# Kernel tuning notes

Hardware: AMD Instinct MI355X
Metric: run time of the kernel (lower is better)

## Reference

```python
import jax, jax.numpy as jnp
import numpy as np

# Static discretization grid (torch version computes this on host from data;
# with inputs in [0,1) the clamps min(..,-2)-0.1 / max(..,2)+0.1 make it constant).
PPU = 128          # points_per_unit
MULT = 16          # 2 ** rho.num_halving_layers
XMIN, XMAX = -2.1, 2.1
NUM_GRID = int(np.ceil(PPU * (XMAX - XMIN) / MULT) * MULT)  # 544
SIGMA_CH = 1024
RHO_C = 8          # rho in/out channels


def setup_inputs() -> dict:
    key = jax.random.key(0)
    ks = jax.random.split(key, 8)
    B, N, M = 8, 2048, 2048
    log_ls = float(np.log(2.0 / PPU))  # init_length_scale = 2 / points_per_unit
    return {
        "x": jax.random.uniform(ks[0], (B, N, 1), dtype=jnp.float32),
        "y": jax.random.normal(ks[1], (B, N, 1), dtype=jnp.float32),
        "x_out": jax.random.uniform(ks[2], (B, M, 1), dtype=jnp.float32),
        # encoder ConvDeepSet (in_channels = 2: density + y)
        "enc_sigma": jnp.full((2,), log_ls, dtype=jnp.float32),
        "enc_W": jax.random.normal(ks[3], (2, RHO_C), dtype=jnp.float32) * 0.5,
        "enc_b": jnp.zeros((RHO_C,), dtype=jnp.float32),
        # rho stand-in: point-wise linear 8 -> 8
        "rho_W": jax.random.normal(ks[4], (RHO_C, RHO_C), dtype=jnp.float32) * 0.35,
        "rho_b": jnp.zeros((RHO_C,), dtype=jnp.float32),
        # mean FinalLayer (in_channels = rho.out_channels = 8, out_channels = 1)
        "mean_sigma": jnp.full((RHO_C,), log_ls, dtype=jnp.float32),
        "mean_W": jax.random.normal(ks[5], (RHO_C, 1), dtype=jnp.float32) * 0.35,
        "mean_b": jnp.zeros((1,), dtype=jnp.float32),
        # sigma FinalLayer (out_channels = sigma_channels = 1024)
        "sig_sigma": jnp.full((RHO_C,), log_ls, dtype=jnp.float32),
        "sig_W": jax.random.normal(ks[6], (RHO_C, SIGMA_CH), dtype=jnp.float32) * 0.35,
        "sig_b": jnp.zeros((SIGMA_CH,), dtype=jnp.float32),
        "noise_scale": jnp.zeros((1,), dtype=jnp.float32),
    }


def _rbf_weights(a, t, log_sigma):
    # a: (B, n, 1), t: (B, m, 1) -> (B, n, m, C) per-channel RBF weights
    d = (a - jnp.swapaxes(t, 1, 2)) ** 2            # (B, n, m) squared dists
    scales = jnp.exp(log_sigma)                      # (C,)
    return jnp.exp(-0.5 * d[..., None] / scales ** 2)


def reference(x, y, x_out, enc_sigma, enc_W, enc_b, rho_W, rho_b,
              mean_sigma, mean_W, mean_b, sig_sigma, sig_W, sig_b, noise_scale):
    B = x.shape[0]
    grid = jnp.broadcast_to(
        jnp.linspace(XMIN, XMAX, NUM_GRID, dtype=x.dtype)[None, :, None],
        (B, NUM_GRID, 1))

    # --- encoder ConvDeepSet: density channel + value channel, RBF smoothing onto grid
    wt = _rbf_weights(x, grid, enc_sigma)            # (B, N, G, 2)
    y_aug = jnp.concatenate([jnp.ones_like(x), y], axis=-1)  # (B, N, 2)
    F = jnp.einsum('bnc,bngc->bgc', y_aug, wt)       # (B, G, 2)
    den, conv = F[..., :1], F[..., 1:]
    F = jnp.concatenate([den, conv / (den + 1e-8)], axis=-1)
    h = jax.nn.sigmoid(F @ enc_W + enc_b)            # (B, G, 8)

    # --- rho (stand-in point-wise linear CNN)
    h = h @ rho_W + rho_b                            # (B, G, 8)

    # --- mean FinalLayer: RBF set-conv from grid to x_out, then linear
    wt_m = _rbf_weights(grid, x_out, mean_sigma)     # (B, G, M, 8)
    mean = jnp.einsum('bgc,bgmc->bmc', h, wt_m) @ mean_W + mean_b  # (B, M, 1)

    # --- sigma FinalLayer -> basis embedding, inner-product covariance
    wt_s = _rbf_weights(grid, x_out, sig_sigma)      # (B, G, M, 8)
    basis = jnp.einsum('bgc,bgmc->bmc', h, wt_s) @ sig_W + sig_b   # (B, M, 1024)
    cov = jnp.einsum('bmc,bnc->bmn', basis, basis)   # (B, M, M)
    cov = cov + jnp.exp(noise_scale[0]) * jnp.eye(cov.shape[-1], dtype=cov.dtype)
    return mean, cov
```

## Files before the change

kernel.cpp:

```cpp
#include <hip/hip_runtime.h>
#include <math.h>

#define GRID_N 544
#define BATCH  8
#define NPTS   2048
#define MPTS   2048
#define XMIN_F (-2.1f)
#define STEP_F (4.2f / 543.0f)

#define PRM_OFF 0
#define H_OFF   128
#define FS_OFF  (H_OFF + BATCH*GRID_N*8)
#define P_OFF   (FS_OFF + BATCH*MPTS*8)
#define CM_OFF  (P_OFF + BATCH*MPTS*8)

__global__ __launch_bounds__(256) void k_params(
    const float* __restrict__ enc_sigma, const float* __restrict__ mean_sigma,
    const float* __restrict__ sig_sigma, const float* __restrict__ sig_W,
    const float* __restrict__ sig_b, const float* __restrict__ noise_scale,
    float* __restrict__ prm) {
  int t = threadIdx.x;
  __shared__ float part[256];
  {
    int pair = t >> 2, q = t & 3;
    int i = pair >> 3, j = pair & 7;
    float s = 0.f;
    int k0 = q * 256;
    for (int k = k0; k < k0 + 256; ++k) s += sig_W[i*1024+k] * sig_W[j*1024+k];
    part[t] = s;
    __syncthreads();
    if (q == 0) prm[24 + pair] = part[t] + part[t+1] + part[t+2] + part[t+3];
    __syncthreads();
  }
  {
    int ch = t >> 5, lane = t & 31;
    float s = 0.f;
    for (int k = lane; k < 1024; k += 32) s += sig_W[ch*1024+k] * sig_b[k];
    part[t] = s;
    __syncthreads();
    if (lane == 0) {
      float acc = 0.f;
      for (int k = 0; k < 32; ++k) acc += part[(ch<<5)+k];
      prm[88 + ch] = acc;
    }
    __syncthreads();
  }
  if (t < 32) {
    float v = 0.f;
    for (int k = t; k < 1024; k += 32) v += sig_b[k] * sig_b[k];
    part[t] = v;
  }
  __syncthreads();
  if (t == 0) {
    float v = 0.f;
    for (int k = 0; k < 32; ++k) v += part[k];
    prm[96] = v;
    prm[97] = __expf(noise_scale[0]);
  } else if (t == 1) {
    prm[0] = 0.5f * __expf(-2.f * enc_sigma[0]);
    prm[1] = 0.5f * __expf(-2.f * enc_sigma[1]);
    prm[98] = (enc_sigma[0] == enc_sigma[1]) ? 1.f : 0.f;
    bool mu = true, su = true;
    for (int c = 0; c < 8; ++c) {
      prm[8 + c]  = 0.5f * __expf(-2.f * mean_sigma[c]);
      prm[16 + c] = 0.5f * __expf(-2.f * sig_sigma[c]);
      if (mean_sigma[c] != mean_sigma[0]) mu = false;
      if (sig_sigma[c]  != sig_sigma[0])  su = false;
    }
    prm[99]  = mu ? 1.f : 0.f;
    prm[100] = su ? 1.f : 0.f;
    prm[101] = (mu && su && mean_sigma[0] == sig_sigma[0]) ? 1.f : 0.f;
  }
}

__global__ __launch_bounds__(256) void k_encode(
    const float* __restrict__ x, const float* __restrict__ y,
    const float* __restrict__ enc_W, const float* __restrict__ enc_b,
    const float* __restrict__ rho_W, const float* __restrict__ rho_b,
    const float* __restrict__ prm, float* __restrict__ h_out) {
  int b = blockIdx.y, g = blockIdx.x, t = threadIdx.x;
  float gv = XMIN_F + (float)g * STEP_F;
  float a0 = prm[0], a1 = prm[1];
  bool uni = prm[98] != 0.f;
  const float4* x4 = (const float4*)(x + (size_t)b * NPTS);
  const float4* y4 = (const float4*)(y + (size_t)b * NPTS);
  float s0 = 0.f, s1 = 0.f;
  #pragma unroll
  for (int i = 0; i < 2; ++i) {
    int n = i * 256 + t;
    float4 xv = x4[n], yv = y4[n];
    float dx, d, w;
    dx = xv.x - gv; d = dx*dx; w = __expf(-d*a0); s0 += w;
    s1 += yv.x * (uni ? w : __expf(-d*a1));
    dx = xv.y - gv; d = dx*dx; w = __expf(-d*a0); s0 += w;
    s1 += yv.y * (uni ? w : __expf(-d*a1));
    dx = xv.z - gv; d = dx*dx; w = __expf(-d*a0); s0 += w;
    s1 += yv.z * (uni ? w : __expf(-d*a1));
    dx = xv.w - gv; d = dx*dx; w = __expf(-d*a0); s0 += w;
    s1 += yv.w * (uni ? w : __expf(-d*a1));
  }
  #pragma unroll
  for (int off = 32; off > 0; off >>= 1) {
    s0 += __shfl_down(s0, off);
    s1 += __shfl_down(s1, off);
  }
  __shared__ float w0s[4], w1s[4];
  int wid = t >> 6;
  if ((t & 63) == 0) { w0s[wid] = s0; w1s[wid] = s1; }
  __syncthreads();
  if (t == 0) {
    float den = w0s[0] + w0s[1] + w0s[2] + w0s[3];
    float conv = w1s[0] + w1s[1] + w1s[2] + w1s[3];
    float F0 = den, F1 = conv / (den + 1e-8f);
    float hh[8];
    #pragma unroll
    for (int jj = 0; jj < 8; ++jj) {
      float z = F0 * enc_W[jj] + F1 * enc_W[8 + jj] + enc_b[jj];
      hh[jj] = 1.f / (1.f + __expf(-z));
    }
    #pragma unroll
    for (int jj = 0; jj < 8; ++jj) {
      float v = rho_b[jj];
      #pragma unroll
      for (int ii = 0; ii < 8; ++ii) v += hh[ii] * rho_W[ii*8 + jj];
      h_out[((size_t)b * GRID_N + g) * 8 + jj] = v;
    }
  }
}

__global__ __launch_bounds__(256) void k_feat(
    const float* __restrict__ x_out, const float* __restrict__ mean_W,
    const float* __restrict__ mean_b, const float* __restrict__ prm,
    const float* __restrict__ h, float* __restrict__ mean_out,
    float* __restrict__ fS, float* __restrict__ Pv, float* __restrict__ cm) {
  int b = blockIdx.y, t = threadIdx.x;
  int ml = t & 63, slice = t >> 6;
  int m = blockIdx.x * 64 + ml;
  float xo = x_out[(size_t)b * MPTS + m];
  bool fused = prm[101] != 0.f;
  float accm[8] = {0,0,0,0,0,0,0,0};
  float accs[8] = {0,0,0,0,0,0,0,0};
  const float* hb = h + (size_t)b * GRID_N * 8;
  const float4* h4 = (const float4*)hb;
  int gbase = slice * 136;
  if (fused) {
    float a = prm[8];
    for (int gg = 0; gg < 136; ++gg) {
      int g = gbase + gg;
      float gv = XMIN_F + (float)g * STEP_F;
      float dx = gv - xo;
      float w = __expf(-(dx*dx) * a);
      float4 h0 = h4[g*2], h1 = h4[g*2+1];
      accm[0] += h0.x * w; accm[1] += h0.y * w;
      accm[2] += h0.z * w; accm[3] += h0.w * w;
      accm[4] += h1.x * w; accm[5] += h1.y * w;
      accm[6] += h1.z * w; accm[7] += h1.w * w;
    }
    #pragma unroll
    for (int c = 0; c < 8; ++c) accs[c] = accm[c];
  } else {
    float am[8], asg[8];
    #pragma unroll
    for (int c = 0; c < 8; ++c) { am[c] = prm[8 + c]; asg[c] = prm[16 + c]; }
    for (int gg = 0; gg < 136; ++gg) {
      int g = gbase + gg;
      float gv = XMIN_F + (float)g * STEP_F;
      float dx = gv - xo;
      float d = dx * dx;
      #pragma unroll
      for (int c = 0; c < 8; ++c) {
        float hv = hb[g*8 + c];
        accm[c] += hv * __expf(-d * am[c]);
        accs[c] += hv * __expf(-d * asg[c]);
      }
    }
  }
  __shared__ float red[256 * 17];
  #pragma unroll
  for (int c = 0; c < 8; ++c) { red[t*17 + c] = accm[c]; red[t*17 + 8 + c] = accs[c]; }
  __syncthreads();
  if (t < 64) {
    int mm = blockIdx.x * 64 + t;
    float fm[8], fs[8];
    #pragma unroll
    for (int c = 0; c < 8; ++c) {
      fm[c] = red[t*17+c] + red[(t+64)*17+c] + red[(t+128)*17+c] + red[(t+192)*17+c];
      fs[c] = red[t*17+8+c] + red[(t+64)*17+8+c] + red[(t+128)*17+8+c] + red[(t+192)*17+8+c];
    }
    float mv = mean_b[0];
    #pragma unroll
    for (int c = 0; c < 8; ++c) mv += fm[c] * mean_W[c];
    mean_out[(size_t)b * MPTS + mm] = mv;
    float cmv = prm[96];
    #pragma unroll
    for (int c = 0; c < 8; ++c) cmv += fs[c] * prm[88 + c];
    cm[(size_t)b * MPTS + mm] = cmv;
    size_t base = ((size_t)b * MPTS + mm) * 8;
    #pragma unroll
    for (int c2 = 0; c2 < 8; ++c2) {
      float p = prm[88 + c2];
      #pragma unroll
      for (int c = 0; c < 8; ++c) p += fs[c] * prm[24 + c*8 + c2];
      Pv[base + c2] = p;
    }
    #pragma unroll
    for (int c = 0; c < 8; ++c) fS[base + c] = fs[c];
  }
}

__global__ __launch_bounds__(256) void k_cov(
    const float* __restrict__ fS, const float* __restrict__ Pv,
    const float* __restrict__ cm, const float* __restrict__ prm,
    float* __restrict__ cov) {
  int b = blockIdx.y, t = threadIdx.x;
  int mt = blockIdx.x * 16;
  int n0 = t * 8;
  float fn[8][8];
  const float4* fv = (const float4*)(fS + ((size_t)b * MPTS + n0) * 8);
  #pragma unroll
  for (int j = 0; j < 8; ++j) {
    float4 lo = fv[j*2], hi = fv[j*2+1];
    fn[j][0]=lo.x; fn[j][1]=lo.y; fn[j][2]=lo.z; fn[j][3]=lo.w;
    fn[j][4]=hi.x; fn[j][5]=hi.y; fn[j][6]=hi.z; fn[j][7]=hi.w;
  }
  __shared__ float Ps[16*8];
  __shared__ float Cs[16];
  if (t < 128) Ps[t] = Pv[((size_t)b * MPTS + mt) * 8 + t];
  if (t < 16)  Cs[t] = cm[(size_t)b * MPTS + mt + t];
  float noise = prm[97];
  __syncthreads();
  #pragma unroll 1
  for (int mi = 0; mi < 16; ++mi) {
    float p[8];
    #pragma unroll
    for (int c = 0; c < 8; ++c) p[c] = Ps[mi*8 + c];
    float cc = Cs[mi];
    float o[8];
    #pragma unroll
    for (int j = 0; j < 8; ++j) {
      float acc = cc;
      #pragma unroll
      for (int c = 0; c < 8; ++c) acc += p[c] * fn[j][c];
      o[j] = acc;
    }
    int mg = mt + mi;
    if (mg >= n0 && mg < n0 + 8) o[mg - n0] += noise;
    float4* outp = (float4*)(cov + ((size_t)b * MPTS + mg) * MPTS + n0);
    outp[0] = make_float4(o[0], o[1], o[2], o[3]);
    outp[1] = make_float4(o[4], o[5], o[6], o[7]);
  }
}

extern "C" void kernel_launch(void* const* d_in, const int* in_sizes, int n_in,
                              void* d_out, int out_size, void* d_ws, size_t ws_size,
                              hipStream_t stream) {
  const float* x          = (const float*)d_in[0];
  const float* y          = (const float*)d_in[1];
  const float* x_out      = (const float*)d_in[2];
  const float* enc_sigma  = (const float*)d_in[3];
  const float* enc_W      = (const float*)d_in[4];
  const float* enc_b      = (const float*)d_in[5];
  const float* rho_W      = (const float*)d_in[6];
  const float* rho_b      = (const float*)d_in[7];
  const float* mean_sigma = (const float*)d_in[8];
  const float* mean_W     = (const float*)d_in[9];
  const float* mean_b     = (const float*)d_in[10];
  const float* sig_sigma  = (const float*)d_in[11];
  const float* sig_W      = (const float*)d_in[12];
  const float* sig_b      = (const float*)d_in[13];
  const float* noise_sc   = (const float*)d_in[14];

  float* wsf = (float*)d_ws;
  float* prm = wsf + PRM_OFF;
  float* hbuf = wsf + H_OFF;
  float* fSb = wsf + FS_OFF;
  float* Pb  = wsf + P_OFF;
  float* cmb = wsf + CM_OFF;

  float* mean_out = (float*)d_out;
  float* cov_out  = mean_out + (size_t)BATCH * MPTS;

  k_params<<<1, 256, 0, stream>>>(enc_sigma, mean_sigma, sig_sigma,
                                  sig_W, sig_b, noise_sc, prm);
  k_encode<<<dim3(GRID_N, BATCH), 256, 0, stream>>>(x, y, enc_W, enc_b,
                                                    rho_W, rho_b, prm, hbuf);
  k_feat<<<dim3(MPTS/64, BATCH), 256, 0, stream>>>(x_out, mean_W, mean_b, prm,
                                                   hbuf, mean_out, fSb, Pb, cmb);
  k_cov<<<dim3(MPTS/16, BATCH), 256, 0, stream>>>(fSb, Pb, cmb, prm, cov_out);
}
```

Before: 221.9 us.

## Fold params kernel into encode, split feat grid finer, coalesce cov row stores

Removes the single-block k_params launch by computing its work in an extra block of k_encode, and computes encoder scales inline. k_feat now uses 32 outputs per block with 8 grid slices, doubling the block count, and skips writing the duplicate sigma partial sums when the bandwidths match. k_cov changes each thread's columns from 8 contiguous to two groups of 4 so that float4 row stores are coalesced across threads. The main cost targeted is the store pattern of the large covariance output, plus one kernel launch. In exchange there is a small register-layout change and a k_feat reduction with more partial sums.

```diff
diff --git a/kernel.cpp b/kernel.cpp
--- a/kernel.cpp
+++ b/kernel.cpp
@@ -14,74 +14,71 @@
 #define P_OFF   (FS_OFF + BATCH*MPTS*8)
 #define CM_OFF  (P_OFF + BATCH*MPTS*8)
 
-__global__ __launch_bounds__(256) void k_params(
-    const float* __restrict__ enc_sigma, const float* __restrict__ mean_sigma,
-    const float* __restrict__ sig_sigma, const float* __restrict__ sig_W,
-    const float* __restrict__ sig_b, const float* __restrict__ noise_scale,
-    float* __restrict__ prm) {
-  int t = threadIdx.x;
-  __shared__ float part[256];
-  {
-    int pair = t >> 2, q = t & 3;
-    int i = pair >> 3, j = pair & 7;
-    float s = 0.f;
-    int k0 = q * 256;
-    for (int k = k0; k < k0 + 256; ++k) s += sig_W[i*1024+k] * sig_W[j*1024+k];
-    part[t] = s;
-    __syncthreads();
-    if (q == 0) prm[24 + pair] = part[t] + part[t+1] + part[t+2] + part[t+3];
-    __syncthreads();
-  }
-  {
-    int ch = t >> 5, lane = t & 31;
-    float s = 0.f;
-    for (int k = lane; k < 1024; k += 32) s += sig_W[ch*1024+k] * sig_b[k];
-    part[t] = s;
-    __syncthreads();
-    if (lane == 0) {
-      float acc = 0.f;
-      for (int k = 0; k < 32; ++k) acc += part[(ch<<5)+k];
-      prm[88 + ch] = acc;
-    }
-    __syncthreads();
-  }
-  if (t < 32) {
-    float v = 0.f;
-    for (int k = t; k < 1024; k += 32) v += sig_b[k] * sig_b[k];
-    part[t] = v;
-  }
-  __syncthreads();
-  if (t == 0) {
-    float v = 0.f;
-    for (int k = 0; k < 32; ++k) v += part[k];
-    prm[96] = v;
-    prm[97] = __expf(noise_scale[0]);
-  } else if (t == 1) {
-    prm[0] = 0.5f * __expf(-2.f * enc_sigma[0]);
-    prm[1] = 0.5f * __expf(-2.f * enc_sigma[1]);
-    prm[98] = (enc_sigma[0] == enc_sigma[1]) ? 1.f : 0.f;
-    bool mu = true, su = true;
-    for (int c = 0; c < 8; ++c) {
-      prm[8 + c]  = 0.5f * __expf(-2.f * mean_sigma[c]);
-      prm[16 + c] = 0.5f * __expf(-2.f * sig_sigma[c]);
-      if (mean_sigma[c] != mean_sigma[0]) mu = false;
-      if (sig_sigma[c]  != sig_sigma[0])  su = false;
-    }
-    prm[99]  = mu ? 1.f : 0.f;
-    prm[100] = su ? 1.f : 0.f;
-    prm[101] = (mu && su && mean_sigma[0] == sig_sigma[0]) ? 1.f : 0.f;
-  }
-}
-
 __global__ __launch_bounds__(256) void k_encode(
     const float* __restrict__ x, const float* __restrict__ y,
+    const float* __restrict__ enc_sigma,
     const float* __restrict__ enc_W, const float* __restrict__ enc_b,
     const float* __restrict__ rho_W, const float* __restrict__ rho_b,
-    const float* __restrict__ prm, float* __restrict__ h_out) {
+    const float* __restrict__ mean_sigma, const float* __restrict__ sig_sigma,
+    const float* __restrict__ sig_W, const float* __restrict__ sig_b,
+    float* __restrict__ prm, float* __restrict__ h_out) {
   int b = blockIdx.y, g = blockIdx.x, t = threadIdx.x;
+
+  if (g == GRID_N) {
+    if (b != 0) return;
+    __shared__ float part[256];
+    {
+      int pair = t >> 2, q = t & 3;
+      int i = pair >> 3, j = pair & 7;
+      float s = 0.f;
+      int k0 = q * 256;
+      for (int k = k0; k < k0 + 256; ++k) s += sig_W[i*1024+k] * sig_W[j*1024+k];
+      part[t] = s;
+      __syncthreads();
+      if (q == 0) prm[16 + pair] = part[t] + part[t+1] + part[t+2] + part[t+3];
+      __syncthreads();
+    }
+    {
+      int ch = t >> 5, lane = t & 31;
+      float s = 0.f;
+      for (int k = lane; k < 1024; k += 32) s += sig_W[ch*1024+k] * sig_b[k];
+      part[t] = s;
+      __syncthreads();
+      if (lane == 0) {
+        float acc = 0.f;
+        for (int k = 0; k < 32; ++k) acc += part[(ch<<5)+k];
+        prm[80 + ch] = acc;
+      }
+      __syncthreads();
+    }
+    if (t < 32) {
+      float v = 0.f;
+      for (int k = t; k < 1024; k += 32) v += sig_b[k] * sig_b[k];
+      part[t] = v;
+    }
+    __syncthreads();
+    if (t == 0) {
+      float v = 0.f;
+      for (int k = 0; k < 32; ++k) v += part[k];
+      prm[88] = v;
+    } else if (t == 1) {
+      bool f = true;
+      for (int c = 0; c < 8; ++c) {
+        prm[c]     = 0.5f * __expf(-2.f * mean_sigma[c]);
+        prm[8 + c] = 0.5f * __expf(-2.f * sig_sigma[c]);
+        if (mean_sigma[c] != mean_sigma[0] || sig_sigma[c] != sig_sigma[0]) f = false;
+      }
+      if (mean_sigma[0] != sig_sigma[0]) f = false;
+      prm[89] = f ? 1.f : 0.f;
+    }
+    return;
+  }
+
   float gv = XMIN_F + (float)g * STEP_F;
-  float a0 = prm[0], a1 = prm[1];
-  bool uni = prm[98] != 0.f;
+  float es0 = enc_sigma[0], es1 = enc_sigma[1];
+  float a0 = 0.5f * __expf(-2.f * es0);
+  float a1 = 0.5f * __expf(-2.f * es1);
+  bool uni = (es0 == es1);
   const float4* x4 = (const float4*)(x + (size_t)b * NPTS);
   const float4* y4 = (const float4*)(y + (size_t)b * NPTS);
   float s0 = 0.f, s1 = 0.f;
@@ -134,18 +131,18 @@
     const float* __restrict__ h, float* __restrict__ mean_out,
     float* __restrict__ fS, float* __restrict__ Pv, float* __restrict__ cm) {
   int b = blockIdx.y, t = threadIdx.x;
-  int ml = t & 63, slice = t >> 6;
-  int m = blockIdx.x * 64 + ml;
+  int ml = t & 31, slice = t >> 5;
+  int m = blockIdx.x * 32 + ml;
   float xo = x_out[(size_t)b * MPTS + m];
-  bool fused = prm[101] != 0.f;
+  bool fused = prm[89] != 0.f;
   float accm[8] = {0,0,0,0,0,0,0,0};
   float accs[8] = {0,0,0,0,0,0,0,0};
   const float* hb = h + (size_t)b * GRID_N * 8;
   const float4* h4 = (const float4*)hb;
-  int gbase = slice * 136;
+  int gbase = slice * 68;
   if (fused) {
-    float a = prm[8];
-    for (int gg = 0; gg < 136; ++gg) {
+    float a = prm[0];
+    for (int gg = 0; gg < 68; ++gg) {
       int g = gbase + gg;
       float gv = XMIN_F + (float)g * STEP_F;
       float dx = gv - xo;
@@ -156,13 +153,11 @@
       accm[4] += h1.x * w; accm[5] += h1.y * w;
       accm[6] += h1.z * w; accm[7] += h1.w * w;
     }
-    #pragma unroll
-    for (int c = 0; c < 8; ++c) accs[c] = accm[c];
   } else {
     float am[8], asg[8];
     #pragma unroll
-    for (int c = 0; c < 8; ++c) { am[c] = prm[8 + c]; asg[c] = prm[16 + c]; }
-    for (int gg = 0; gg < 136; ++gg) {
+    for (int c = 0; c < 8; ++c) { am[c] = prm[c]; asg[c] = prm[8 + c]; }
+    for (int gg = 0; gg < 68; ++gg) {
       int g = gbase + gg;
       float gv = XMIN_F + (float)g * STEP_F;
       float dx = gv - xo;
@@ -177,30 +172,47 @@
   }
   __shared__ float red[256 * 17];
   #pragma unroll
-  for (int c = 0; c < 8; ++c) { red[t*17 + c] = accm[c]; red[t*17 + 8 + c] = accs[c]; }
+  for (int c = 0; c < 8; ++c) {
+    red[t*17 + c] = accm[c];
+    if (!fused) red[t*17 + 8 + c] = accs[c];
+  }
   __syncthreads();
-  if (t < 64) {
-    int mm = blockIdx.x * 64 + t;
+  if (t < 32) {
+    int mm = blockIdx.x * 32 + t;
     float fm[8], fs[8];
     #pragma unroll
     for (int c = 0; c < 8; ++c) {
-      fm[c] = red[t*17+c] + red[(t+64)*17+c] + red[(t+128)*17+c] + red[(t+192)*17+c];
-      fs[c] = red[t*17+8+c] + red[(t+64)*17+8+c] + red[(t+128)*17+8+c] + red[(t+192)*17+8+c];
+      float v = 0.f;
+      #pragma unroll
+      for (int s = 0; s < 8; ++s) v += red[(t + 32*s)*17 + c];
+      fm[c] = v;
+    }
+    if (fused) {
+      #pragma unroll
+      for (int c = 0; c < 8; ++c) fs[c] = fm[c];
+    } else {
+      #pragma unroll
+      for (int c = 0; c < 8; ++c) {
+        float v = 0.f;
+        #pragma unroll
+        for (int s = 0; s < 8; ++s) v += red[(t + 32*s)*17 + 8 + c];
+        fs[c] = v;
+      }
     }
     float mv = mean_b[0];
     #pragma unroll
     for (int c = 0; c < 8; ++c) mv += fm[c] * mean_W[c];
     mean_out[(size_t)b * MPTS + mm] = mv;
-    float cmv = prm[96];
-    #pragma unroll
-    for (int c = 0; c < 8; ++c) cmv += fs[c] * prm[88 + c];
+    float cmv = prm[88];
+    #pragma unroll
+    for (int c = 0; c < 8; ++c) cmv += fs[c] * prm[80 + c];
     cm[(size_t)b * MPTS + mm] = cmv;
     size_t base = ((size_t)b * MPTS + mm) * 8;
     #pragma unroll
     for (int c2 = 0; c2 < 8; ++c2) {
-      float p = prm[88 + c2];
-      #pragma unroll
-      for (int c = 0; c < 8; ++c) p += fs[c] * prm[24 + c*8 + c2];
+      float p = prm[80 + c2];
+      #pragma unroll
+      for (int c = 0; c < 8; ++c) p += fs[c] * prm[16 + c*8 + c2];
       Pv[base + c2] = p;
     }
     #pragma unroll
@@ -210,24 +222,27 @@
 
 __global__ __launch_bounds__(256) void k_cov(
     const float* __restrict__ fS, const float* __restrict__ Pv,
-    const float* __restrict__ cm, const float* __restrict__ prm,
+    const float* __restrict__ cm, const float* __restrict__ noise_scale,
     float* __restrict__ cov) {
   int b = blockIdx.y, t = threadIdx.x;
   int mt = blockIdx.x * 16;
-  int n0 = t * 8;
-  float fn[8][8];
-  const float4* fv = (const float4*)(fS + ((size_t)b * MPTS + n0) * 8);
+  float noise = __expf(noise_scale[0]);
+  float fa[4][8], fb[4][8];
+  const float4* fva = (const float4*)(fS + ((size_t)b * MPTS + 4*t) * 8);
+  const float4* fvb = (const float4*)(fS + ((size_t)b * MPTS + 1024 + 4*t) * 8);
   #pragma unroll
-  for (int j = 0; j < 8; ++j) {
-    float4 lo = fv[j*2], hi = fv[j*2+1];
-    fn[j][0]=lo.x; fn[j][1]=lo.y; fn[j][2]=lo.z; fn[j][3]=lo.w;
-    fn[j][4]=hi.x; fn[j][5]=hi.y; fn[j][6]=hi.z; fn[j][7]=hi.w;
+  for (int j = 0; j < 4; ++j) {
+    float4 lo = fva[j*2], hi = fva[j*2+1];
+    fa[j][0]=lo.x; fa[j][1]=lo.y; fa[j][2]=lo.z; fa[j][3]=lo.w;
+    fa[j][4]=hi.x; fa[j][5]=hi.y; fa[j][6]=hi.z; fa[j][7]=hi.w;
+    float4 lo2 = fvb[j*2], hi2 = fvb[j*2+1];
+    fb[j][0]=lo2.x; fb[j][1]=lo2.y; fb[j][2]=lo2.z; fb[j][3]=lo2.w;
+    fb[j][4]=hi2.x; fb[j][5]=hi2.y; fb[j][6]=hi2.z; fb[j][7]=hi2.w;
   }
   __shared__ float Ps[16*8];
   __shared__ float Cs[16];
   if (t < 128) Ps[t] = Pv[((size_t)b * MPTS + mt) * 8 + t];
   if (t < 16)  Cs[t] = cm[(size_t)b * MPTS + mt + t];
-  float noise = prm[97];
   __syncthreads();
   #pragma unroll 1
   for (int mi = 0; mi < 16; ++mi) {
@@ -235,19 +250,20 @@
     #pragma unroll
     for (int c = 0; c < 8; ++c) p[c] = Ps[mi*8 + c];
     float cc = Cs[mi];
-    float o[8];
-    #pragma unroll
-    for (int j = 0; j < 8; ++j) {
-      float acc = cc;
-      #pragma unroll
-      for (int c = 0; c < 8; ++c) acc += p[c] * fn[j][c];
-      o[j] = acc;
-    }
     int mg = mt + mi;
-    if (mg >= n0 && mg < n0 + 8) o[mg - n0] += noise;
-    float4* outp = (float4*)(cov + ((size_t)b * MPTS + mg) * MPTS + n0);
-    outp[0] = make_float4(o[0], o[1], o[2], o[3]);
-    outp[1] = make_float4(o[4], o[5], o[6], o[7]);
+    float oa[4], ob[4];
+    #pragma unroll
+    for (int j = 0; j < 4; ++j) {
+      float acc = cc, acc2 = cc;
+      #pragma unroll
+      for (int c = 0; c < 8; ++c) { acc += p[c] * fa[j][c]; acc2 += p[c] * fb[j][c]; }
+      if (mg == 4*t + j)        acc  += noise;
+      if (mg == 1024 + 4*t + j) acc2 += noise;
+      oa[j] = acc; ob[j] = acc2;
+    }
+    float4* r = (float4*)(cov + ((size_t)b * MPTS + mg) * MPTS);
+    r[t]       = make_float4(oa[0], oa[1], oa[2], oa[3]);
+    r[256 + t] = make_float4(ob[0], ob[1], ob[2], ob[3]);
   }
 }
 
@@ -271,20 +287,19 @@
   const float* noise_sc   = (const float*)d_in[14];
 
   float* wsf = (float*)d_ws;
-  float* prm = wsf + PRM_OFF;
+  float* prm  = wsf + PRM_OFF;
   float* hbuf = wsf + H_OFF;
-  float* fSb = wsf + FS_OFF;
-  float* Pb  = wsf + P_OFF;
-  float* cmb = wsf + CM_OFF;
+  float* fSb  = wsf + FS_OFF;
+  float* Pb   = wsf + P_OFF;
+  float* cmb  = wsf + CM_OFF;
 
   float* mean_out = (float*)d_out;
   float* cov_out  = mean_out + (size_t)BATCH * MPTS;
 
-  k_params<<<1, 256, 0, stream>>>(enc_sigma, mean_sigma, sig_sigma,
-                                  sig_W, sig_b, noise_sc, prm);
-  k_encode<<<dim3(GRID_N, BATCH), 256, 0, stream>>>(x, y, enc_W, enc_b,
-                                                    rho_W, rho_b, prm, hbuf);
-  k_feat<<<dim3(MPTS/64, BATCH), 256, 0, stream>>>(x_out, mean_W, mean_b, prm,
+  k_encode<<<dim3(GRID_N + 1, BATCH), 256, 0, stream>>>(
+      x, y, enc_sigma, enc_W, enc_b, rho_W, rho_b,
+      mean_sigma, sig_sigma, sig_W, sig_b, prm, hbuf);
+  k_feat<<<dim3(MPTS/32, BATCH), 256, 0, stream>>>(x_out, mean_W, mean_b, prm,
                                                    hbuf, mean_out, fSb, Pb, cmb);
-  k_cov<<<dim3(MPTS/16, BATCH), 256, 0, stream>>>(fSb, Pb, cmb, prm, cov_out);
+  k_cov<<<dim3(MPTS/16, BATCH), 256, 0, stream>>>(fSb, Pb, cmb, noise_sc, cov_out);
 }
```

Result: slower. 231.6 us (+4.4%).
